# Performance work log

Hardware: AMD Instinct MI355X
Metric: run time of the kernel (lower is better)

## Reference

```python
import jax, jax.numpy as jnp
import numpy as np
from itertools import combinations

N = 8192
F_FACES = 16384
D_IN = 64
D_OUT = 64
EPS = 1e-07


def setup_inputs() -> dict:
    key = jax.random.key(0)
    ks = jax.random.split(key, 8)
    inp = {
        "input": jax.random.normal(ks[0], (1, N, D_IN), dtype=jnp.float32),
        "A": jnp.zeros((1, 1), dtype=jnp.float32),  # unused by the module
        "Dinv": jax.random.uniform(ks[1], (1, N, 1), dtype=jnp.float32),  # overwritten by the module
        "vertices": jax.random.normal(ks[2], (1, N, 3), dtype=jnp.float32),
        "faces": jax.random.randint(ks[3], (1, F_FACES, 3), 0, N, dtype=jnp.int64),
        "sigma": jnp.full((1,), 0.1, dtype=jnp.float32),
        "fc_w": jax.random.normal(ks[4], (D_OUT, D_IN), dtype=jnp.float32) / np.sqrt(D_IN),
        "fc_b": jnp.zeros((D_OUT,), dtype=jnp.float32),
        "nfc_w": jax.random.normal(ks[5], (D_OUT, D_IN), dtype=jnp.float32) / np.sqrt(D_IN),
        "nfc_b": jnp.zeros((D_OUT,), dtype=jnp.float32),
    }
    return inp


def reference(input, A, Dinv, vertices, faces, sigma, fc_w, fc_b, nfc_w, nfc_b):
    B, n, D = vertices.shape  # D == 3
    # directed edges among the D=3 face vertex slots: 6 ordered pairs
    halfedges = np.array(list(combinations(range(D), 2)), dtype=np.int32)  # (3, 2)
    edges = np.concatenate([halfedges, halfedges[:, ::-1]], axis=0)  # (6, 2)
    # gather per-face endpoint vertex indices: (F, 6, 2) -> (E, 2)
    all_edges = faces[0][:, edges].reshape(-1, 2)  # int, values in [0, n)
    src, dst = all_edges[:, 0], all_edges[:, 1]
    # edge weight: exp(-||v_src - v_dst||^2 / sigma^2)
    d2 = jnp.sum((vertices[0, src] - vertices[0, dst]) ** 2, axis=1)  # (E,)
    w = jnp.exp(-d2 / (sigma[0] ** 2))
    # scatter into dense n x n (duplicate edges carry identical weights -> set is well-defined)
    dist = jnp.zeros((n, n), dtype=jnp.float32).at[src, dst].set(w)
    dist = jnp.maximum(dist, EPS)
    # torch sums over dim=1 of (1, n, n) -> column sums; row i scaled by 1/colsum[i]
    dinv = 1.0 / jnp.sum(dist, axis=0)  # (n,)
    coeff = dinv[:, None] * dist  # (n, n)
    y = jnp.einsum('bni,oi->bno', input, fc_w) + fc_b
    y_neigh = coeff @ input[0]  # (n, d_in), B == 1
    y_neigh = jnp.einsum('ni,oi->no', y_neigh, nfc_w) + nfc_b
    return y + y_neigh[None]
```

## Files before the change

kernel.cpp:

```cpp
#include <hip/hip_runtime.h>

#define N_V 8192
#define NFACES 16384
#define NEDGES (NFACES * 6)
#define D 64
#define EPS 1e-7f
#define HASH_CAP 262144u

__global__ void total_sum_kernel(const float* __restrict__ input, float* __restrict__ total) {
    int col = threadIdx.x & 63;
    int rq  = threadIdx.x >> 6;
    int rowBase = blockIdx.x * 256;
    float s = 0.f;
    for (int r = rq; r < 256; r += 4)
        s += input[(size_t)(rowBase + r) * D + col];
    atomicAdd(&total[col], s);
}

__global__ void edge_kernel(const int* __restrict__ faces,
                            const float* __restrict__ verts,
                            const float* __restrict__ input,
                            const float* __restrict__ sigma,
                            unsigned* __restrict__ htab,
                            float* __restrict__ rowacc,
                            float* __restrict__ colsum) {
    int e = blockIdx.x * blockDim.x + threadIdx.x;
    if (e >= NEDGES) return;
    int f = e / 6, s = e % 6;
    const int p0[6] = {0, 0, 1, 1, 2, 2};
    const int p1[6] = {1, 2, 2, 0, 0, 1};
    int a = faces[f * 3 + p0[s]];
    int b = faces[f * 3 + p1[s]];

    float dx = verts[a * 3 + 0] - verts[b * 3 + 0];
    float dy = verts[a * 3 + 1] - verts[b * 3 + 1];
    float dz = verts[a * 3 + 2] - verts[b * 3 + 2];
    float d2 = dx * dx + dy * dy + dz * dz;
    float sg = sigma[0];
    float w  = expf(-d2 / (sg * sg));
    float wp = fmaxf(w, EPS) - EPS;
    if (wp <= 0.f) return;

    unsigned key = ((unsigned)a << 13) | (unsigned)b;
    unsigned h = (key * 2654435761u) & (HASH_CAP - 1u);
    while (true) {
        unsigned prev = atomicCAS(&htab[h], 0xFFFFFFFFu, key);
        if (prev == key) return;
        if (prev == 0xFFFFFFFFu) break;
        h = (h + 1u) & (HASH_CAP - 1u);
    }

    atomicAdd(&colsum[b], wp);
    const float* inb = input + (size_t)b * D;
    float* ra = rowacc + (size_t)a * D;
#pragma unroll
    for (int k = 0; k < D; ++k)
        atomicAdd(&ra[k], wp * inb[k]);
}

__global__ __launch_bounds__(256) void final_kernel(
        const float* __restrict__ input,
        const float* __restrict__ rowacc,
        const float* __restrict__ colsum,
        const float* __restrict__ total,
        const float* __restrict__ fc_w, const float* __restrict__ fc_b,
        const float* __restrict__ nfc_w, const float* __restrict__ nfc_b,
        float* __restrict__ out) {
    __shared__ float wfc[D][D + 1];
    __shared__ float wnf[D][D + 1];
    __shared__ float rin[4][D];
    __shared__ float zz[4][D];
    __shared__ float bias[D];
    __shared__ float etot[D];

    for (int i = threadIdx.x; i < D * D; i += 256) {
        wfc[i >> 6][i & 63] = fc_w[i];
        wnf[i >> 6][i & 63] = nfc_w[i];
    }
    if (threadIdx.x < D) {
        bias[threadIdx.x] = fc_b[threadIdx.x] + nfc_b[threadIdx.x];
        etot[threadIdx.x] = EPS * total[threadIdx.x];
    }
    __syncthreads();

    const int rl = threadIdx.x >> 6;
    const int o  = threadIdx.x & 63;
    const int rowsPerBlock = N_V / gridDim.x;
    const int row0 = blockIdx.x * rowsPerBlock;
    const float nEps = (float)N_V * EPS;

    for (int rr = 0; rr < rowsPerBlock; rr += 4) {
        int row = row0 + rr + rl;
        rin[rl][o] = input[(size_t)row * D + o];
        float dinv = 1.f / (nEps + colsum[row]);
        zz[rl][o] = dinv * (etot[o] + rowacc[(size_t)row * D + o]);
        __syncthreads();
        float acc = bias[o];
#pragma unroll
        for (int k = 0; k < D; ++k)
            acc += rin[rl][k] * wfc[o][k] + zz[rl][k] * wnf[o][k];
        out[(size_t)row * D + o] = acc;
        __syncthreads();
    }
}

extern "C" void kernel_launch(void* const* d_in, const int* in_sizes, int n_in,
                              void* d_out, int out_size, void* d_ws, size_t ws_size,
                              hipStream_t stream) {
    const float* input    = (const float*)d_in[0];
    const float* vertices = (const float*)d_in[3];
    const int*   faces    = (const int*)d_in[4];
    const float* sigma    = (const float*)d_in[5];
    const float* fc_w     = (const float*)d_in[6];
    const float* fc_b     = (const float*)d_in[7];
    const float* nfc_w    = (const float*)d_in[8];
    const float* nfc_b    = (const float*)d_in[9];
    float* out = (float*)d_out;

    unsigned* htab = (unsigned*)d_ws;
    float* rowacc  = (float*)d_ws + HASH_CAP;
    float* colsum  = rowacc + (size_t)N_V * D;
    float* total   = colsum + N_V;

    hipMemsetAsync(htab, 0xFF, HASH_CAP * sizeof(unsigned), stream);
    hipMemsetAsync(rowacc, 0, ((size_t)N_V * D + N_V + D) * sizeof(float), stream);

    total_sum_kernel<<<32, 256, 0, stream>>>(input, total);
    edge_kernel<<<(NEDGES + 255) / 256, 256, 0, stream>>>(faces, vertices, input, sigma,
                                                          htab, rowacc, colsum);
    final_kernel<<<256, 256, 0, stream>>>(input, rowacc, colsum, total,
                                          fc_w, fc_b, nfc_w, nfc_b, out);
}
```

Before: 42.16 us.

## Fuse workspace init into setup kernel and process edges per face

Replaces the two memset calls and the atomic column-sum kernel with a single setup kernel. That kernel zeroes the accumulators, initialises the hash table and writes per-block partial sums, which the edge kernel then reduces. The edge kernel now runs one thread per face: it loads the three vertices once and computes three weights, each shared by both edge directions. The hash table is shrunk to 8192 slots, which assumes only a few edges survive the weight threshold. If many more edges survive, the table can fill up and the probe loop would never end.

```diff
diff --git a/kernel.cpp b/kernel.cpp
--- a/kernel.cpp
+++ b/kernel.cpp
@@ -2,45 +2,44 @@
 
 #define N_V 8192
 #define NFACES 16384
-#define NEDGES (NFACES * 6)
 #define D 64
 #define EPS 1e-7f
-#define HASH_CAP 262144u
+#define HASH_CAP 8192u
 
-__global__ void total_sum_kernel(const float* __restrict__ input, float* __restrict__ total) {
-    int col = threadIdx.x & 63;
-    int rq  = threadIdx.x >> 6;
-    int rowBase = blockIdx.x * 256;
+
+__global__ __launch_bounds__(256) void setup_kernel(const float* __restrict__ input,
+                                                    unsigned* __restrict__ htab,
+                                                    float* __restrict__ rowacc,
+                                                    float* __restrict__ colsum,
+                                                    float* __restrict__ totpart) {
+    const int tid = blockIdx.x * 256 + threadIdx.x;
+
+    float4* ra4 = (float4*)rowacc;
+    const float4 z4 = make_float4(0.f, 0.f, 0.f, 0.f);
+    for (int i = tid; i < N_V * D / 4; i += 16384) ra4[i] = z4;
+    if (tid < N_V) colsum[tid] = 0.f;
+    if (tid < (int)HASH_CAP) htab[tid] = 0xFFFFFFFFu;
+
+    const int col = threadIdx.x & 63;
+    const int rq  = threadIdx.x >> 6;
+    const int rowBase = blockIdx.x * 128;
     float s = 0.f;
-    for (int r = rq; r < 256; r += 4)
+    for (int r = rq; r < 128; r += 4)
         s += input[(size_t)(rowBase + r) * D + col];
-    atomicAdd(&total[col], s);
+    __shared__ float sh[4][D];
+    sh[rq][col] = s;
+    __syncthreads();
+    if (threadIdx.x < D)
+        totpart[blockIdx.x * D + threadIdx.x] =
+            sh[0][threadIdx.x] + sh[1][threadIdx.x] + sh[2][threadIdx.x] + sh[3][threadIdx.x];
 }
 
-__global__ void edge_kernel(const int* __restrict__ faces,
-                            const float* __restrict__ verts,
-                            const float* __restrict__ input,
-                            const float* __restrict__ sigma,
-                            unsigned* __restrict__ htab,
-                            float* __restrict__ rowacc,
-                            float* __restrict__ colsum) {
-    int e = blockIdx.x * blockDim.x + threadIdx.x;
-    if (e >= NEDGES) return;
-    int f = e / 6, s = e % 6;
-    const int p0[6] = {0, 0, 1, 1, 2, 2};
-    const int p1[6] = {1, 2, 2, 0, 0, 1};
-    int a = faces[f * 3 + p0[s]];
-    int b = faces[f * 3 + p1[s]];
-
-    float dx = verts[a * 3 + 0] - verts[b * 3 + 0];
-    float dy = verts[a * 3 + 1] - verts[b * 3 + 1];
-    float dz = verts[a * 3 + 2] - verts[b * 3 + 2];
-    float d2 = dx * dx + dy * dy + dz * dz;
-    float sg = sigma[0];
-    float w  = expf(-d2 / (sg * sg));
-    float wp = fmaxf(w, EPS) - EPS;
+__device__ __forceinline__ void process_edge(int a, int b, float wp,
+                                             unsigned* __restrict__ htab,
+                                             float* __restrict__ rowacc,
+                                             float* __restrict__ colsum,
+                                             const float* __restrict__ input) {
     if (wp <= 0.f) return;
-
     unsigned key = ((unsigned)a << 13) | (unsigned)b;
     unsigned h = (key * 2654435761u) & (HASH_CAP - 1u);
     while (true) {
@@ -49,7 +48,6 @@
         if (prev == 0xFFFFFFFFu) break;
         h = (h + 1u) & (HASH_CAP - 1u);
     }
-
     atomicAdd(&colsum[b], wp);
     const float* inb = input + (size_t)b * D;
     float* ra = rowacc + (size_t)a * D;
@@ -58,11 +56,55 @@
         atomicAdd(&ra[k], wp * inb[k]);
 }
 
+__global__ __launch_bounds__(256) void edge_kernel(const int* __restrict__ faces,
+                                                   const float* __restrict__ verts,
+                                                   const float* __restrict__ input,
+                                                   const float* __restrict__ sigma,
+                                                   unsigned* __restrict__ htab,
+                                                   float* __restrict__ rowacc,
+                                                   float* __restrict__ colsum,
+                                                   const float* __restrict__ totpart,
+                                                   float* __restrict__ etot) {
+    if (blockIdx.x == 0 && threadIdx.x < D) {
+        float s = 0.f;
+#pragma unroll 8
+        for (int j = 0; j < 64; ++j) s += totpart[j * D + threadIdx.x];
+        etot[threadIdx.x] = EPS * s;
+    }
+
+    const int f = blockIdx.x * 256 + threadIdx.x;
+    const int a = faces[3 * f + 0];
+    const int b = faces[3 * f + 1];
+    const int c = faces[3 * f + 2];
+
+    const float ax = verts[3 * a], ay = verts[3 * a + 1], az = verts[3 * a + 2];
+    const float bx = verts[3 * b], by = verts[3 * b + 1], bz = verts[3 * b + 2];
+    const float cx = verts[3 * c], cy = verts[3 * c + 1], cz = verts[3 * c + 2];
+
+    const float sg = sigma[0];
+    const float inv_s2 = 1.f / (sg * sg);
+
+    float dx, dy, dz;
+    dx = ax - bx; dy = ay - by; dz = az - bz;
+    const float wab = fmaxf(expf(-(dx * dx + dy * dy + dz * dz) * inv_s2), EPS) - EPS;
+    dx = ax - cx; dy = ay - cy; dz = az - cz;
+    const float wac = fmaxf(expf(-(dx * dx + dy * dy + dz * dz) * inv_s2), EPS) - EPS;
+    dx = bx - cx; dy = by - cy; dz = bz - cz;
+    const float wbc = fmaxf(expf(-(dx * dx + dy * dy + dz * dz) * inv_s2), EPS) - EPS;
+
+    process_edge(a, b, wab, htab, rowacc, colsum, input);
+    process_edge(b, a, wab, htab, rowacc, colsum, input);
+    process_edge(a, c, wac, htab, rowacc, colsum, input);
+    process_edge(c, a, wac, htab, rowacc, colsum, input);
+    process_edge(b, c, wbc, htab, rowacc, colsum, input);
+    process_edge(c, b, wbc, htab, rowacc, colsum, input);
+}
+
 __global__ __launch_bounds__(256) void final_kernel(
         const float* __restrict__ input,
         const float* __restrict__ rowacc,
         const float* __restrict__ colsum,
-        const float* __restrict__ total,
+        const float* __restrict__ etot_g,
         const float* __restrict__ fc_w, const float* __restrict__ fc_b,
         const float* __restrict__ nfc_w, const float* __restrict__ nfc_b,
         float* __restrict__ out) {
@@ -79,7 +121,7 @@
     }
     if (threadIdx.x < D) {
         bias[threadIdx.x] = fc_b[threadIdx.x] + nfc_b[threadIdx.x];
-        etot[threadIdx.x] = EPS * total[threadIdx.x];
+        etot[threadIdx.x] = etot_g[threadIdx.x];
     }
     __syncthreads();
 
@@ -120,14 +162,12 @@
     unsigned* htab = (unsigned*)d_ws;
     float* rowacc  = (float*)d_ws + HASH_CAP;
     float* colsum  = rowacc + (size_t)N_V * D;
-    float* total   = colsum + N_V;
+    float* totpart = colsum + N_V;
+    float* etot    = totpart + 64 * 64;
 
-    hipMemsetAsync(htab, 0xFF, HASH_CAP * sizeof(unsigned), stream);
-    hipMemsetAsync(rowacc, 0, ((size_t)N_V * D + N_V + D) * sizeof(float), stream);
-
-    total_sum_kernel<<<32, 256, 0, stream>>>(input, total);
-    edge_kernel<<<(NEDGES + 255) / 256, 256, 0, stream>>>(faces, vertices, input, sigma,
-                                                          htab, rowacc, colsum);
-    final_kernel<<<256, 256, 0, stream>>>(input, rowacc, colsum, total,
+    setup_kernel<<<64, 256, 0, stream>>>(input, htab, rowacc, colsum, totpart);
+    edge_kernel<<<64, 256, 0, stream>>>(faces, vertices, input, sigma,
+                                        htab, rowacc, colsum, totpart, etot);
+    final_kernel<<<256, 256, 0, stream>>>(input, rowacc, colsum, etot,
                                           fc_w, fc_b, nfc_w, nfc_b, out);
 }
```

Measured after the change: 43.42 us. 1.03x slower.
